# Performance work log

Measured on AMD Instinct MI355X. Metric: run time of the kernel, lower is better.

## Reference

```python
import jax, jax.numpy as jnp
import numpy as np

SIGMA = 1.0
SQRT2 = float(np.sqrt(2.0))


def setup_inputs() -> dict:
    key = jax.random.key(0)
    k1, k2 = jax.random.split(key)
    B, L = 128, 1024
    preds = jax.random.normal(k1, (B, L), dtype=jnp.float32)
    # integer relevance grades 0..4, stored as float as in the torch module
    target = jax.random.randint(k2, (B, L), 0, 5).astype(jnp.float32)
    return {"preds": preds, "target": target}


def reference(preds, target):
    B, L = preds.shape
    # pairwise diff [B, L, L]: diff[b,i,j] = preds[b,i] - preds[b,j]
    diff = preds[:, :, None] - preds[:, None, :]
    # Normal(0, sigma*sqrt(2)).cdf(diff) == ndtr(diff / (sigma*sqrt(2)))
    p = jax.scipy.special.ndtr(diff / (SIGMA * SQRT2))
    # zero the diagonal (i == j) before summing
    eye = jnp.eye(L, dtype=bool)
    p = jnp.where(eye[None, :, :], 0.0, p)
    expected_ranks = 1.0 + p.sum(axis=2)  # [B, L]

    gains = 2.0 ** target - 1.0
    discounts = jnp.log2(expected_ranks + 1.0)
    dcg = (gains / discounts).sum(axis=1)  # [B]

    ideal_target = jnp.sort(target, axis=1)[:, ::-1]  # descending
    ideal_gains = 2.0 ** ideal_target - 1.0
    ideal_discounts = jnp.log2(jnp.arange(1, L + 1, dtype=jnp.float32) + 1.0)
    idcg = (ideal_gains / ideal_discounts).sum(axis=1)  # [B]

    ndcg = dcg / (idcg + 1e-10)
    return -ndcg.mean()
```

## Files before the change

### kernel.cpp

```cpp
#include <hip/hip_runtime.h>
#include <hip/hip_fp16.h>

#define B 128
#define L 1024

#if __has_builtin(__builtin_amdgcn_exp2f)
#define EXP2(x) __builtin_amdgcn_exp2f(x)
#else
#define EXP2(x) __expf((x) * 0.6931471805599453f)
#endif

typedef unsigned int uint4v __attribute__((ext_vector_type(4)));
typedef float f32x2 __attribute__((ext_vector_type(2)));

#define WS_ACC  2048
#define WS_GCTR 2049

#define K1f -1.6279072f
#define K2f -0.9299637f
#define K3f -0.1074808f

__device__ __forceinline__ void term2(unsigned int du, __half2 pi2,
                                      __half2 k1, __half2 k2, __half2 k3,
                                      __half2 one2, __half2& acc) {
    __half2 pj = __builtin_bit_cast(__half2, du);
    __half2 d  = __hsub2(pi2, pj);
    unsigned int dbits = __builtin_bit_cast(unsigned int, d);
    __half2 a  = __builtin_bit_cast(__half2, dbits & 0x7fff7fffu);
    __half2 t  = __hfma2(k3, a, k2);
    __half2 u  = __hfma2(t,  a, k1);
    __half2 w  = __hmul2(a, u);
    __half2 e  = __halves2half2(hexp2(__low2half(w)),
                                hexp2(__high2half(w)));
    __half2 r  = __hsub2(one2, e);
    unsigned int rs = (dbits & 0x80008000u)
                    | (__builtin_bit_cast(unsigned int, r) & 0x7fff7fffu);
    acc = __hadd2(acc, __builtin_bit_cast(__half2, rs));
}

__device__ __forceinline__ f32x2 h2f(__half2 h) {
    float2 f = __half22float2(h);
    f32x2 r; r.x = f.x; r.y = f.y;
    return r;
}

__global__ __launch_bounds__(256, 8) void pair_kernel(const float* __restrict__ preds,
                                                      const float* __restrict__ target,
                                                      float* __restrict__ ws) {
    __shared__ __align__(16) __half sph[L];
    __shared__ float red[256];

    const int blk  = blockIdx.x;
    const int b    = blk >> 4;
    const int iseg = blk & 15;
    const int tid  = threadIdx.x;
    const int il   = tid & 63;
    const int jq   = tid >> 6;

    if (blk == 0 && tid == 0) {
        ws[WS_ACC] = 0.0f;
        ((int*)ws)[WS_GCTR] = 0;
    }

    const float* prow = preds + b * L;

    float4 v4 = reinterpret_cast<const float4*>(prow)[tid];
    __half2 h01 = __floats2half2_rn(0.5f * v4.x, 0.5f * v4.y);
    __half2 h23 = __floats2half2_rn(0.5f * v4.z, 0.5f * v4.w);
    reinterpret_cast<__half2*>(sph)[tid * 2 + 0] = h01;
    reinterpret_cast<__half2*>(sph)[tid * 2 + 1] = h23;

    const int i = iseg * 64 + il;
    const float tgt = (tid < 64) ? target[b * L + iseg * 64 + tid] : 0.0f;

    __syncthreads();

    const __half2 pi2  = __half2half2(sph[i]);
    const __half2 k1   = __floats2half2_rn(K1f, K1f);
    const __half2 k2   = __floats2half2_rn(K2f, K2f);
    const __half2 k3   = __floats2half2_rn(K3f, K3f);
    const __half2 one2 = __floats2half2_rn(1.0f, 1.0f);
    const __half2 z2   = __floats2half2_rn(0.0f, 0.0f);

    const uint4v* basep = reinterpret_cast<const uint4v*>(sph + jq * 256);

    float E = 0.0f;
    for (int wdw = 0; wdw < 2; ++wdw) {
        __half2 A0 = z2, A1 = z2, A2 = z2, A3 = z2,
                A4 = z2, A5 = z2, A6 = z2, A7 = z2;
        #pragma unroll
        for (int m = 0; m < 8; ++m) {
            uint4v q0 = basep[wdw * 16 + m * 2 + 0];
            uint4v q1 = basep[wdw * 16 + m * 2 + 1];
            term2(q0.x, pi2, k1, k2, k3, one2, A0);
            term2(q0.y, pi2, k1, k2, k3, one2, A1);
            term2(q0.z, pi2, k1, k2, k3, one2, A2);
            term2(q0.w, pi2, k1, k2, k3, one2, A3);
            term2(q1.x, pi2, k1, k2, k3, one2, A4);
            term2(q1.y, pi2, k1, k2, k3, one2, A5);
            term2(q1.z, pi2, k1, k2, k3, one2, A6);
            term2(q1.w, pi2, k1, k2, k3, one2, A7);
        }
        f32x2 s01 = (h2f(A0) + h2f(A1)) + (h2f(A2) + h2f(A3));
        f32x2 s45 = (h2f(A4) + h2f(A5)) + (h2f(A6) + h2f(A7));
        f32x2 s   = s01 + s45;
        E += s.x + s.y;
    }

    red[tid] = E;
    __syncthreads();

    if (tid < 64) {
        float Es = (red[tid] + red[tid + 64]) + (red[tid + 128] + red[tid + 192]);
        float er1 = 513.5f + 0.5f * Es;
        float g = EXP2(tgt) - 1.0f;
        float contrib = g * __builtin_amdgcn_rcpf(__log2f(er1));
        #pragma unroll
        for (int off = 32; off > 0; off >>= 1)
            contrib += __shfl_down(contrib, off);
        if (tid == 0)
            ws[blk] = contrib;
    }
}

__global__ __launch_bounds__(256) void finish_kernel(const float* __restrict__ target,
                                                     float* __restrict__ ws,
                                                     float* __restrict__ out) {
    __shared__ unsigned long long cred[256];
    __shared__ float2 fred[256];

    const int b   = blockIdx.x;
    const int tid = threadIdx.x;
    const float* trow = target + b * L;

    unsigned long long cnt = 0ull;
    #pragma unroll
    for (int k = 0; k < 4; ++k) {
        float t = trow[tid + k * 256];
        cnt += ((unsigned long long)(t > 3.5f) << 48)
             + ((unsigned long long)(t > 2.5f) << 32)
             + ((unsigned long long)(t > 1.5f) << 16)
             + ((unsigned long long)(t > 0.5f));
    }
    cred[tid] = cnt;
    __syncthreads();
    #pragma unroll
    for (int s = 128; s > 0; s >>= 1) {
        if (tid < (unsigned)s) cred[tid] += cred[tid + s];
        __syncthreads();
    }
    unsigned long long tot = cred[0];
    const int n4 = (int)(tot >> 48) & 0xFFFF;
    const int n3 = (int)(tot >> 32) & 0xFFFF;
    const int n2 = (int)(tot >> 16) & 0xFFFF;
    const int n1 = (int)(tot)       & 0xFFFF;

    float idcg_p = 0.0f;
    #pragma unroll
    for (int k = 0; k < 4; ++k) {
        int pos = tid + 1 + k * 256;
        float gain = (pos <= n4) ? 15.0f : (pos <= n3) ? 7.0f :
                     (pos <= n2) ? 3.0f  : (pos <= n1) ? 1.0f : 0.0f;
        idcg_p += gain * __builtin_amdgcn_rcpf(__log2f((float)pos + 1.0f));
    }
    float dcg_p = (tid < 16) ? ws[b * 16 + tid] : 0.0f;
    fred[tid] = make_float2(idcg_p, dcg_p);
    __syncthreads();
    #pragma unroll
    for (int s = 128; s > 0; s >>= 1) {
        if (tid < (unsigned)s) {
            float2 x = fred[tid], y = fred[tid + s];
            fred[tid] = make_float2(x.x + y.x, x.y + y.y);
        }
        __syncthreads();
    }

    if (tid == 0) {
        float ndcg = fred[0].y / (fred[0].x + 1e-10f);
        atomicAdd(&ws[WS_ACC], ndcg);
        __threadfence();
        int old = atomicAdd((int*)ws + WS_GCTR, 1);
        if (old == B - 1) {
            float acc = atomicAdd(&ws[WS_ACC], 0.0f);
            out[0] = -acc * (1.0f / (float)B);
        }
    }
}

extern "C" void kernel_launch(void* const* d_in, const int* in_sizes, int n_in,
                              void* d_out, int out_size, void* d_ws, size_t ws_size,
                              hipStream_t stream) {
    const float* preds  = (const float*)d_in[0];
    const float* target = (const float*)d_in[1];
    float* out = (float*)d_out;
    float* ws  = (float*)d_ws;

    pair_kernel<<<B * 16, 256, 0, stream>>>(preds, target, ws);
    finish_kernel<<<B, 256, 0, stream>>>(target, ws, out);
}
```

Before: 86.67 us.

## Exploit pairwise antisymmetry to compute only upper-triangle tiles

Uses the odd symmetry of the centred erf-like term, term(i,j) = -term(j,i), so only the upper-triangular 64x64 tiles are evaluated. Each tile produces row partial sums, and column partial sums for off-diagonal tiles, which are written to the workspace. The finish kernel then gathers them to rebuild each row's expected rank. This roughly halves the transcendental work but adds workspace traffic, more LDS reductions, a serial gather loop in finish_kernel, and uneven per-block work (1 to 8 row strips).

```diff
diff --git a/kernel.cpp b/kernel.cpp
--- a/kernel.cpp
+++ b/kernel.cpp
@@ -3,6 +3,8 @@
 
 #define B 128
 #define L 1024
+#define NTILE 24
+#define TSTRIDE 576
 
 #if __has_builtin(__builtin_amdgcn_exp2f)
 #define EXP2(x) __builtin_amdgcn_exp2f(x)
@@ -11,18 +13,17 @@
 #endif
 
 typedef unsigned int uint4v __attribute__((ext_vector_type(4)));
-typedef float f32x2 __attribute__((ext_vector_type(2)));
-
-#define WS_ACC  2048
-#define WS_GCTR 2049
+
+#define WS_ACC  (B * NTILE * TSTRIDE)
+#define WS_GCTR (WS_ACC + 1)
 
 #define K1f -1.6279072f
 #define K2f -0.9299637f
 #define K3f -0.1074808f
 
-__device__ __forceinline__ void term2(unsigned int du, __half2 pi2,
-                                      __half2 k1, __half2 k2, __half2 k3,
-                                      __half2 one2, __half2& acc) {
+__device__ __forceinline__ __half2 term2v(unsigned int du, __half2 pi2,
+                                          __half2 k1, __half2 k2, __half2 k3,
+                                          __half2 one2) {
     __half2 pj = __builtin_bit_cast(__half2, du);
     __half2 d  = __hsub2(pi2, pj);
     unsigned int dbits = __builtin_bit_cast(unsigned int, d);
@@ -35,27 +36,26 @@
     __half2 r  = __hsub2(one2, e);
     unsigned int rs = (dbits & 0x80008000u)
                     | (__builtin_bit_cast(unsigned int, r) & 0x7fff7fffu);
-    acc = __hadd2(acc, __builtin_bit_cast(__half2, rs));
-}
-
-__device__ __forceinline__ f32x2 h2f(__half2 h) {
-    float2 f = __half22float2(h);
-    f32x2 r; r.x = f.x; r.y = f.y;
-    return r;
+    return __builtin_bit_cast(__half2, rs);
 }
 
 __global__ __launch_bounds__(256, 8) void pair_kernel(const float* __restrict__ preds,
                                                       const float* __restrict__ target,
                                                       float* __restrict__ ws) {
-    __shared__ __align__(16) __half sph[L];
-    __shared__ float red[256];
-
-    const int blk  = blockIdx.x;
-    const int b    = blk >> 4;
-    const int iseg = blk & 15;
-    const int tid  = threadIdx.x;
-    const int il   = tid & 63;
-    const int jq   = tid >> 6;
+    __shared__ __align__(16) unsigned char smem[2048 + 8192 + 8192];
+    __half* sph = (__half*)smem;
+    float* rowLDS = (float*)(smem + 2048);
+    unsigned int* colLDS = (unsigned int*)(smem + 2048 + 8192);
+    float* col2LDS = (float*)smem;
+
+    const int blk = blockIdx.x;
+    const int b   = blk / NTILE;
+    const int tl  = blk - b * NTILE;
+    const int r   = (tl >= 16) ? 1 : 0;
+    const int q   = r ? (tl - 8) : tl;
+    const int tid = threadIdx.x;
+    const int il  = tid & 63;
+    const int jq  = tid >> 6;
 
     if (blk == 0 && tid == 0) {
         ws[WS_ACC] = 0.0f;
@@ -63,63 +63,77 @@
     }
 
     const float* prow = preds + b * L;
-
     float4 v4 = reinterpret_cast<const float4*>(prow)[tid];
-    __half2 h01 = __floats2half2_rn(0.5f * v4.x, 0.5f * v4.y);
-    __half2 h23 = __floats2half2_rn(0.5f * v4.z, 0.5f * v4.w);
-    reinterpret_cast<__half2*>(sph)[tid * 2 + 0] = h01;
-    reinterpret_cast<__half2*>(sph)[tid * 2 + 1] = h23;
-
-    const int i = iseg * 64 + il;
-    const float tgt = (tid < 64) ? target[b * L + iseg * 64 + tid] : 0.0f;
-
-    __syncthreads();
-
-    const __half2 pi2  = __half2half2(sph[i]);
+    reinterpret_cast<__half2*>(sph)[tid * 2 + 0] = __floats2half2_rn(0.5f * v4.x, 0.5f * v4.y);
+    reinterpret_cast<__half2*>(sph)[tid * 2 + 1] = __floats2half2_rn(0.5f * v4.z, 0.5f * v4.w);
+    __syncthreads();
+
     const __half2 k1   = __floats2half2_rn(K1f, K1f);
     const __half2 k2   = __floats2half2_rn(K2f, K2f);
     const __half2 k3   = __floats2half2_rn(K3f, K3f);
     const __half2 one2 = __floats2half2_rn(1.0f, 1.0f);
     const __half2 z2   = __floats2half2_rn(0.0f, 0.0f);
 
-    const uint4v* basep = reinterpret_cast<const uint4v*>(sph + jq * 256);
-
-    float E = 0.0f;
-    for (int wdw = 0; wdw < 2; ++wdw) {
-        __half2 A0 = z2, A1 = z2, A2 = z2, A3 = z2,
-                A4 = z2, A5 = z2, A6 = z2, A7 = z2;
+    const uint4v* cp4 = reinterpret_cast<const uint4v*>(sph + q * 64 + jq * 16);
+    uint4v pq0 = cp4[0], pq1 = cp4[1];
+    unsigned int pjb[8] = {pq0.x, pq0.y, pq0.z, pq0.w, pq1.x, pq1.y, pq1.z, pq1.w};
+
+    __half2 colacc[8] = {z2, z2, z2, z2, z2, z2, z2, z2};
+
+    const int r8 = r << 3;
+    for (int rr = 0; rr < 8; ++rr) {
+        const int s = r8 + rr;
+        if (s > q) break;
+        const bool ca = (s < q);
+        const __half2 pi2 = __half2half2(sph[(s << 6) + il]);
+        __half2 A = z2, Bc = z2;
         #pragma unroll
         for (int m = 0; m < 8; ++m) {
-            uint4v q0 = basep[wdw * 16 + m * 2 + 0];
-            uint4v q1 = basep[wdw * 16 + m * 2 + 1];
-            term2(q0.x, pi2, k1, k2, k3, one2, A0);
-            term2(q0.y, pi2, k1, k2, k3, one2, A1);
-            term2(q0.z, pi2, k1, k2, k3, one2, A2);
-            term2(q0.w, pi2, k1, k2, k3, one2, A3);
-            term2(q1.x, pi2, k1, k2, k3, one2, A4);
-            term2(q1.y, pi2, k1, k2, k3, one2, A5);
-            term2(q1.z, pi2, k1, k2, k3, one2, A6);
-            term2(q1.w, pi2, k1, k2, k3, one2, A7);
-        }
-        f32x2 s01 = (h2f(A0) + h2f(A1)) + (h2f(A2) + h2f(A3));
-        f32x2 s45 = (h2f(A4) + h2f(A5)) + (h2f(A6) + h2f(A7));
-        f32x2 s   = s01 + s45;
-        E += s.x + s.y;
-    }
-
-    red[tid] = E;
+            __half2 tm = term2v(pjb[m], pi2, k1, k2, k3, one2);
+            if (m < 4) A = __hadd2(A, tm); else Bc = __hadd2(Bc, tm);
+            if (ca) colacc[m] = __hadd2(colacc[m], tm);
+        }
+        float2 fA = __half22float2(A), fB = __half22float2(Bc);
+        rowLDS[(rr << 8) + (jq << 6) + il] = (fA.x + fA.y) + (fB.x + fB.y);
+    }
+
+    #pragma unroll
+    for (int m = 0; m < 8; ++m)
+        colLDS[((jq << 3) + m) * 64 + il] = __builtin_bit_cast(unsigned int, colacc[m]);
+    __syncthreads();
+
+    float* wst = ws + (b * NTILE + tl) * TSTRIDE;
+
+    #pragma unroll
+    for (int h = 0; h < 2; ++h) {
+        int rho = tid + (h << 8);
+        int rrx = rho >> 6, ilx = rho & 63;
+        float v = (rowLDS[(rrx << 8) + ilx]       + rowLDS[(rrx << 8) + 64 + ilx])
+                + (rowLDS[(rrx << 8) + 128 + ilx] + rowLDS[(rrx << 8) + 192 + ilx]);
+        wst[rho] = v;
+    }
+
+    {
+        int cp = tid & 31, ilq = tid >> 5;
+        const uint4v* cl = reinterpret_cast<const uint4v*>(colLDS + cp * 64 + ilq * 8);
+        uint4v c0 = cl[0], c1 = cl[1];
+        unsigned int cc[8] = {c0.x, c0.y, c0.z, c0.w, c1.x, c1.y, c1.z, c1.w};
+        float sx = 0.0f, sy = 0.0f;
+        #pragma unroll
+        for (int k = 0; k < 8; ++k) {
+            float2 f = __half22float2(__builtin_bit_cast(__half2, cc[k]));
+            sx += f.x; sy += f.y;
+        }
+        col2LDS[ilq * 64 + cp * 2 + 0] = sx;
+        col2LDS[ilq * 64 + cp * 2 + 1] = sy;
+    }
     __syncthreads();
 
     if (tid < 64) {
-        float Es = (red[tid] + red[tid + 64]) + (red[tid + 128] + red[tid + 192]);
-        float er1 = 513.5f + 0.5f * Es;
-        float g = EXP2(tgt) - 1.0f;
-        float contrib = g * __builtin_amdgcn_rcpf(__log2f(er1));
+        float cs = 0.0f;
         #pragma unroll
-        for (int off = 32; off > 0; off >>= 1)
-            contrib += __shfl_down(contrib, off);
-        if (tid == 0)
-            ws[blk] = contrib;
+        for (int g = 0; g < 8; ++g) cs += col2LDS[g * 64 + tid];
+        wst[512 + tid] = cs;
     }
 }
 
@@ -133,10 +147,12 @@
     const int tid = threadIdx.x;
     const float* trow = target + b * L;
 
+    float tv[4];
     unsigned long long cnt = 0ull;
     #pragma unroll
     for (int k = 0; k < 4; ++k) {
         float t = trow[tid + k * 256];
+        tv[k] = t;
         cnt += ((unsigned long long)(t > 3.5f) << 48)
              + ((unsigned long long)(t > 2.5f) << 32)
              + ((unsigned long long)(t > 1.5f) << 16)
@@ -163,7 +179,28 @@
                      (pos <= n2) ? 3.0f  : (pos <= n1) ? 1.0f : 0.0f;
         idcg_p += gain * __builtin_amdgcn_rcpf(__log2f((float)pos + 1.0f));
     }
-    float dcg_p = (tid < 16) ? ws[b * 16 + tid] : 0.0f;
+
+    const int b24 = b * NTILE;
+    float dcg_p = 0.0f;
+    #pragma unroll
+    for (int k = 0; k < 4; ++k) {
+        int i  = tid + (k << 8);
+        int u  = i >> 6;
+        int rb = u >> 3;
+        int rho = i & 511;
+        float rowsum = 0.0f;
+        for (int qq = u; qq < 16; ++qq)
+            rowsum += ws[(b24 + qq + (rb << 3)) * TSTRIDE + rho];
+        float cols = 0.0f;
+        int i6 = i & 63;
+        if (u >= 1) cols += ws[(b24 + u) * TSTRIDE + 512 + i6];
+        if (u >= 9) cols += ws[(b24 + u + 8) * TSTRIDE + 512 + i6];
+        float Es  = rowsum - cols;
+        float er1 = 513.5f + 0.5f * Es;
+        float g   = EXP2(tv[k]) - 1.0f;
+        dcg_p += g * __builtin_amdgcn_rcpf(__log2f(er1));
+    }
+
     fred[tid] = make_float2(idcg_p, dcg_p);
     __syncthreads();
     #pragma unroll
@@ -195,6 +232,6 @@
     float* out = (float*)d_out;
     float* ws  = (float*)d_ws;
 
-    pair_kernel<<<B * 16, 256, 0, stream>>>(preds, target, ws);
+    pair_kernel<<<B * NTILE, 256, 0, stream>>>(preds, target, ws);
     finish_kernel<<<B, 256, 0, stream>>>(target, ws, out);
 }
```

Result: slower. 95.44 us (+10.1%).
